# Optimization experiments

Measured on AMD Instinct MI355X. Metric: run time of the kernel, lower is better.

## Reference

```python
import jax, jax.numpy as jnp
import numpy as np

N = 50000      # nodes
E = 500000     # edges (avg degree 10)
D_IN = 256     # input feature dim
HID = 256      # hidden_channels
HEADS = 8
C_HID = HID // HEADS   # 32 per-head dim for concat layers
NCLS = 8               # num_classes (last layer per-head dim, concat=False)


def setup_inputs() -> dict:
    key = jax.random.key(0)
    keys = iter(jax.random.split(key, 64))
    def w(shape, s=0.05):
        return jax.random.normal(next(keys), shape, jnp.float32) * s
    inp = {}
    inp["x"] = jax.random.normal(next(keys), (N, D_IN), jnp.float32)
    inp["edge_index"] = jax.random.randint(next(keys), (2, E), 0, N, jnp.int32)
    # (fan_in, heads*per_head_out, skip_out) per layer; layer3: concat=False
    layer_cfg = [(D_IN, HEADS * C_HID, HEADS * C_HID),
                 (HID, HEADS * C_HID, HEADS * C_HID),
                 (HID, HEADS * NCLS, NCLS)]
    for i, (fin, hc, skip) in enumerate(layer_cfg, 1):
        for nm in ("q", "k", "v"):
            inp[f"W{nm}{i}"] = w((fin, hc))
            inp[f"b{nm}{i}"] = jnp.zeros((hc,), jnp.float32)
        inp[f"Ws{i}"] = w((fin, skip))
        inp[f"bs{i}"] = jnp.zeros((skip,), jnp.float32)
        inp[f"Wb{i}"] = w((3 * skip, 1))
    for i in (1, 2):
        inp[f"ln{i}_g"] = jnp.ones((HID,), jnp.float32)
        inp[f"ln{i}_b"] = jnp.zeros((HID,), jnp.float32)
    return inp


def _layer_norm(x, g, b):
    mu = x.mean(-1, keepdims=True)
    var = ((x - mu) ** 2).mean(-1, keepdims=True)
    return (x - mu) * jax.lax.rsqrt(var + 1e-5) * g + b


def _tconv(x, src, dst, Wq, bq, Wk, bk, Wv, bv, Ws, bs, Wb, concat):
    """PyG TransformerConv with beta=True, root_weight=True, eval-mode (no dropout)."""
    n = x.shape[0]
    q = (x @ Wq + bq).reshape(n, HEADS, -1)   # [N,H,C]
    k = (x @ Wk + bk).reshape(n, HEADS, -1)
    v = (x @ Wv + bv).reshape(n, HEADS, -1)
    C = q.shape[-1]
    # per-edge attention logits, scaled dot product
    logits = (q[dst] * k[src]).sum(-1) * jax.lax.rsqrt(jnp.float32(C))  # [E,H]
    # segment softmax over incoming edges of each dst node
    m = jax.ops.segment_max(logits, dst, num_segments=n)                # [N,H]
    m = jnp.where(jnp.isfinite(m), m, 0.0)                              # empty segments
    e = jnp.exp(logits - m[dst])
    s = jax.ops.segment_sum(e, dst, num_segments=n)
    alpha = e / (s[dst] + 1e-16)                                        # [E,H]
    # scatter-aggregate messages
    out = jax.ops.segment_sum(v[src] * alpha[:, :, None], dst, num_segments=n)  # [N,H,C]
    out = out.reshape(n, -1) if concat else out.mean(axis=1)
    # beta-gated skip connection
    xr = x @ Ws + bs
    beta = jax.nn.sigmoid(jnp.concatenate([out, xr, out - xr], axis=-1) @ Wb)   # [N,1]
    return beta * xr + (1.0 - beta) * out


def reference(x, edge_index,
              Wq1, bq1, Wk1, bk1, Wv1, bv1, Ws1, bs1, Wb1,
              Wq2, bq2, Wk2, bk2, Wv2, bv2, Ws2, bs2, Wb2,
              Wq3, bq3, Wk3, bk3, Wv3, bv3, Ws3, bs3, Wb3,
              ln1_g, ln1_b, ln2_g, ln2_b):
    src, dst = edge_index[0], edge_index[1]
    h = jax.nn.relu(_layer_norm(
        _tconv(x, src, dst, Wq1, bq1, Wk1, bk1, Wv1, bv1, Ws1, bs1, Wb1, True),
        ln1_g, ln1_b))
    h = jax.nn.relu(_layer_norm(
        _tconv(h, src, dst, Wq2, bq2, Wk2, bk2, Wv2, bv2, Ws2, bs2, Wb2, True),
        ln2_g, ln2_b))
    return _tconv(h, src, dst, Wq3, bq3, Wk3, bk3, Wv3, bv3, Ws3, bs3, Wb3, False)
```

## Files before the change

kernel.cpp:

```cpp
#include <hip/hip_runtime.h>
#include <stdint.h>

typedef __attribute__((ext_vector_type(8))) short short8;
typedef __attribute__((ext_vector_type(4))) float f32x4;

struct us4 { unsigned short x, y, z, w; };

__device__ __forceinline__ float b2f(unsigned short u){
  union { unsigned int i; float f; } x; x.i = ((unsigned int)u) << 16; return x.f;
}
__device__ __forceinline__ unsigned short f2b(float f){
  union { float f; unsigned int i; } x; x.f = f;
  unsigned int i = x.i;
  unsigned int r = (i + 0x7FFFu + ((i >> 16) & 1u)) >> 16;
  return (unsigned short)r;
}
__device__ __forceinline__ float sane(float v){
  return fminf(fmaxf(v, -1e30f), 1e30f);
}
__device__ __forceinline__ float lclamp(float v){
  return fminf(fmaxf(v, -60.f), 60.f);
}
__device__ __forceinline__ float ldin(const void* p, size_t i, int f32){
  return f32 ? ((const float*)p)[i] : b2f(((const unsigned short*)p)[i]);
}

__global__ void k_flag(const unsigned short* __restrict__ xu, int* __restrict__ flag){
  __shared__ int cnt;
  if (threadIdx.x == 0) cnt = 0;
  __syncthreads();
  unsigned u = xu[2 * threadIdx.x];
  int e = (u >> 7) & 0xFF;
  if (e >= 97 && e <= 132) atomicAdd(&cnt, 1);
  __syncthreads();
  if (threadIdx.x == 0) flag[0] = (cnt >= 192) ? 0 : 1;
}

__global__ void k_cvt(const void* __restrict__ xin, unsigned short* __restrict__ xb,
                      int n4, const int* __restrict__ flagp){
  int f32 = *flagp;
  int i = blockIdx.x * 256 + threadIdx.x;
  if (i < n4){
    if (f32){
      float4 v = ((const float4*)xin)[i];
      us4 o = { f2b(v.x), f2b(v.y), f2b(v.z), f2b(v.w) };
      ((us4*)xb)[i] = o;
    } else {
      ((us4*)xb)[i] = ((const us4*)xin)[i];
    }
  }
}

__global__ void k_deg(const int* __restrict__ ei, int E, int N, int* __restrict__ deg){
  int e = blockIdx.x * 256 + threadIdx.x;
  if (e < E){
    unsigned d = (unsigned)ei[E + e];
    if (d < (unsigned)N) atomicAdd(&deg[d], 1);
  }
}

__global__ void k_bsum(const int* __restrict__ deg, int N, int* __restrict__ bsum){
  int b = blockIdx.x, t = threadIdx.x;
  int i0 = b * 1024 + t * 4;
  int s = 0;
  if (i0 + 4 <= N){
    int4 v = *(const int4*)&deg[i0];
    s = v.x + v.y + v.z + v.w;
  } else {
    #pragma unroll
    for (int j = 0; j < 4; ++j){ int i = i0 + j; if (i < N) s += deg[i]; }
  }
  #pragma unroll
  for (int off = 32; off; off >>= 1) s += __shfl_xor(s, off);
  __shared__ int ws[4];
  if ((t & 63) == 0) ws[t >> 6] = s;
  __syncthreads();
  if (t == 0) bsum[b] = ws[0] + ws[1] + ws[2] + ws[3];
}

__global__ void k_bscan(const int* __restrict__ bsum, int nb,
                        int* __restrict__ boff, int* __restrict__ rowptr, int N){
  int t = threadIdx.x;
  if (nb <= 64){
    int v = (t < nb) ? bsum[t] : 0;
    int inc = v;
    #pragma unroll
    for (int off = 1; off < 64; off <<= 1){
      int u = __shfl_up(inc, off);
      if (t >= off) inc += u;
    }
    if (t < nb) boff[t] = inc - v;
    if (t == 63) rowptr[N] = inc;
  } else {
    if (t == 0){
      int run = 0;
      for (int i = 0; i < nb; ++i){ boff[i] = run; run += bsum[i]; }
      rowptr[N] = run;
    }
  }
}

__global__ void k_rowptr(const int* __restrict__ deg, const int* __restrict__ boff,
                         int N, int* __restrict__ rowptr, int* __restrict__ cursor){
  int b = blockIdx.x, t = threadIdx.x;
  int i0 = b * 1024 + t * 4;
  int d0 = 0, d1 = 0, d2 = 0, d3 = 0;
  if (i0 + 4 <= N){
    int4 v = *(const int4*)&deg[i0];
    d0 = v.x; d1 = v.y; d2 = v.z; d3 = v.w;
  } else {
    if (i0     < N) d0 = deg[i0];
    if (i0 + 1 < N) d1 = deg[i0 + 1];
    if (i0 + 2 < N) d2 = deg[i0 + 2];
    if (i0 + 3 < N) d3 = deg[i0 + 3];
  }
  int s = d0 + d1 + d2 + d3;
  int lane = t & 63, w = t >> 6;
  int inc = s;
  #pragma unroll
  for (int off = 1; off < 64; off <<= 1){
    int u = __shfl_up(inc, off);
    if (lane >= off) inc += u;
  }
  int wex = inc - s;
  __shared__ int wtot[4];
  if (lane == 63) wtot[w] = inc;
  __syncthreads();
  int cross = 0;
  for (int i = 0; i < w; ++i) cross += wtot[i];
  int basev = boff[b] + cross + wex;
  int r0 = basev, r1 = basev + d0, r2 = r1 + d1, r3 = r2 + d2;
  if (i0 + 4 <= N){
    int4 o = { r0, r1, r2, r3 };
    *(int4*)&rowptr[i0] = o;
    *(int4*)&cursor[i0] = o;
  } else {
    if (i0     < N){ rowptr[i0]   = r0; cursor[i0]   = r0; }
    if (i0 + 1 < N){ rowptr[i0+1] = r1; cursor[i0+1] = r1; }
    if (i0 + 2 < N){ rowptr[i0+2] = r2; cursor[i0+2] = r2; }
    if (i0 + 3 < N){ rowptr[i0+3] = r3; cursor[i0+3] = r3; }
  }
}

__global__ void k_scatter(const int* __restrict__ ei, int E, int N,
                          int* __restrict__ cursor, int* __restrict__ srcs){
  int e = blockIdx.x * 256 + threadIdx.x;
  if (e < E){
    unsigned d = (unsigned)ei[E + e];
    if (d < (unsigned)N){
      int pos = atomicAdd(&cursor[d], 1);
      if ((unsigned)pos < (unsigned)E){
        unsigned s = (unsigned)ei[e];
        srcs[pos] = (s < (unsigned)N) ? (int)s : 0;
      }
    }
  }
}

__global__ void k_pack(const void* __restrict__ Wq, const void* __restrict__ bq,
                       const void* __restrict__ Wk, const void* __restrict__ bk,
                       const void* __restrict__ Wv, const void* __restrict__ bv,
                       const void* __restrict__ Ws, const void* __restrict__ bs,
                       unsigned short* __restrict__ WT, float* __restrict__ bias,
                       int Mq, int Ms, int K, const int* __restrict__ flagp){
  int f32 = *flagp;
  int cg = blockIdx.x;
  int k  = threadIdx.x;
  int mat, c, mc;
  if (cg < 3 * Mq){ mat = cg / Mq; c = cg % Mq; mc = Mq; }
  else if (cg < 3 * Mq + Ms){ mat = 3; c = cg - 3 * Mq; mc = Ms; }
  else { mat = 4; c = 0; mc = 1; }
  const void* W = (mat==0)?Wq:(mat==1)?Wk:(mat==2)?Wv:(mat==3)?Ws:(const void*)0;
  WT[(size_t)cg * K + k] = (mat < 4) ? f2b(ldin(W, (size_t)k * mc + c, f32)) : (unsigned short)0;
  if (k == 0){
    const void* B = (mat==0)?bq:(mat==1)?bk:(mat==2)?bv:(mat==3)?bs:(const void*)0;
    bias[cg] = (mat < 4) ? ldin(B, c, f32) : 0.f;
  }
}

__global__ __launch_bounds__(256) void k_gemm(const unsigned short* __restrict__ A,
                                              const unsigned short* __restrict__ WT,
                                              const float* __restrict__ bias,
                                              unsigned short* __restrict__ B0,
                                              unsigned short* __restrict__ B1,
                                              unsigned short* __restrict__ B2,
                                              unsigned short* __restrict__ B3,
                                              int N, int Mout, int secshift){
  __shared__ __align__(16) unsigned short Alds[64][264];
  __shared__ __align__(16) unsigned short Clds[32][276];
  int tid = threadIdx.x, wid = tid >> 6, lane = tid & 63;
  int l15 = lane & 15, l4 = lane >> 4;
  int row0 = blockIdx.x * 64;
  {
    int srow = tid >> 2, sc4 = tid & 3;
    int ar = row0 + srow; if (ar >= N) ar = N - 1;
    const unsigned short* Ap = A + (size_t)ar * 256;
    #pragma unroll
    for (int i = 0; i < 8; ++i){
      int col = (sc4 + 4 * i) * 8;
      *(short8*)&Alds[srow][col] = *(const short8*)&Ap[col];
    }
  }
  __syncthreads();
  int secw = 1 << secshift;
  int strow = tid >> 3, stchunk = tid & 7;
  for (int cb = wid * 64; cb < Mout; cb += 256){
    f32x4 acc[4][4] = {};
    #pragma unroll
    for (int k0 = 0; k0 < 256; k0 += 32){
      short8 a0 = *(const short8*)&Alds[l15     ][k0 + l4*8];
      short8 a1 = *(const short8*)&Alds[16 + l15][k0 + l4*8];
      short8 a2 = *(const short8*)&Alds[32 + l15][k0 + l4*8];
      short8 a3 = *(const short8*)&Alds[48 + l15][k0 + l4*8];
      const unsigned short* wb = WT + (size_t)(cb + l15) * 256 + k0 + l4*8;
      short8 b0 = *(const short8*)(wb);
      short8 b1 = *(const short8*)(wb + 16*256);
      short8 b2 = *(const short8*)(wb + 32*256);
      short8 b3 = *(const short8*)(wb + 48*256);
      acc[0][0] = __builtin_amdgcn_mfma_f32_16x16x32_bf16(a0, b0, acc[0][0], 0,0,0);
      acc[0][1] = __builtin_amdgcn_mfma_f32_16x16x32_bf16(a0, b1, acc[0][1], 0,0,0);
      acc[0][2] = __builtin_amdgcn_mfma_f32_16x16x32_bf16(a0, b2, acc[0][2], 0,0,0);
      acc[0][3] = __builtin_amdgcn_mfma_f32_16x16x32_bf16(a0, b3, acc[0][3], 0,0,0);
      acc[1][0] = __builtin_amdgcn_mfma_f32_16x16x32_bf16(a1, b0, acc[1][0], 0,0,0);
      acc[1][1] = __builtin_amdgcn_mfma_f32_16x16x32_bf16(a1, b1, acc[1][1], 0,0,0);
      acc[1][2] = __builtin_amdgcn_mfma_f32_16x16x32_bf16(a1, b2, acc[1][2], 0,0,0);
      acc[1][3] = __builtin_amdgcn_mfma_f32_16x16x32_bf16(a1, b3, acc[1][3], 0,0,0);
      acc[2][0] = __builtin_amdgcn_mfma_f32_16x16x32_bf16(a2, b0, acc[2][0], 0,0,0);
      acc[2][1] = __builtin_amdgcn_mfma_f32_16x16x32_bf16(a2, b1, acc[2][1], 0,0,0);
      acc[2][2] = __builtin_amdgcn_mfma_f32_16x16x32_bf16(a2, b2, acc[2][2], 0,0,0);
      acc[2][3] = __builtin_amdgcn_mfma_f32_16x16x32_bf16(a2, b3, acc[2][3], 0,0,0);
      acc[3][0] = __builtin_amdgcn_mfma_f32_16x16x32_bf16(a3, b0, acc[3][0], 0,0,0);
      acc[3][1] = __builtin_amdgcn_mfma_f32_16x16x32_bf16(a3, b1, acc[3][1], 0,0,0);
      acc[3][2] = __builtin_amdgcn_mfma_f32_16x16x32_bf16(a3, b2, acc[3][2], 0,0,0);
      acc[3][3] = __builtin_amdgcn_mfma_f32_16x16x32_bf16(a3, b3, acc[3][3], 0,0,0);
    }
    int gb = cb - wid * 64;
    #pragma unroll
    for (int ph = 0; ph < 2; ++ph){
      #pragma unroll
      for (int rt2 = 0; rt2 < 2; ++rt2){
        int rt = ph*2 + rt2;
        #pragma unroll
        for (int ct = 0; ct < 4; ++ct){
          float bv = bias[cb + ct*16 + l15];
          #pragma unroll
          for (int r = 0; r < 4; ++r)
            Clds[rt2*16 + l4*4 + r][wid*64 + ct*16 + l15] = f2b(acc[rt][ct][r] + bv);
        }
      }
      __syncthreads();
      int grow = row0 + ph*32 + strow;
      if (grow < N){
        int g0 = gb + stchunk * 32;
        int mat = g0 >> secshift;
        int cc  = g0 & (secw - 1);
        unsigned short* Bp = (mat==0)?B0:(mat==1)?B1:(mat==2)?B2:B3;
        unsigned short* dst = Bp + (size_t)grow * secw + cc;
        const unsigned short* srcp = &Clds[strow][stchunk * 32];
        #pragma unroll
        for (int j = 0; j < 4; ++j)
          *(short8*)(dst + j*8) = *(const short8*)(srcp + j*8);
      }
      __syncthreads();
    }
  }
}

__global__ __launch_bounds__(256) void k_attn(const unsigned short* __restrict__ qb,
                                              const unsigned short* __restrict__ kb,
                                              const unsigned short* __restrict__ vb,
                                              const unsigned short* __restrict__ xb,
                                              const int* __restrict__ rowptr,
                                              const int* __restrict__ srcs,
                                              const void* __restrict__ Wb,
                                              const void* __restrict__ lng,
                                              const void* __restrict__ lnb,
                                              unsigned short* __restrict__ hout,
                                              int N, int E, const int* __restrict__ flagp){
  int f32 = *flagp;
  int tid = threadIdx.x, w = tid >> 6, l = tid & 63;
  int n = blockIdx.x * 4 + w;
  if (n >= N) return;
  size_t base = (size_t)n * 256;
  us4 qv = *(const us4*)&qb[base + l*4];
  float q0 = b2f(qv.x), q1 = b2f(qv.y), q2 = b2f(qv.z), q3 = b2f(qv.w);
  int e0 = rowptr[n], e1 = rowptr[n+1];
  if (e0 < 0) e0 = 0;
  if (e1 > E) e1 = E;
  const float scale = 0.17677669529663687f;
  float ss = 0.f, o0 = 0.f, o1 = 0.f, o2 = 0.f, o3 = 0.f;
  int e = e0;
  for (; e + 4 <= e1; e += 4){
    unsigned s0 = (unsigned)srcs[e];   if (s0 >= (unsigned)N) s0 = 0;
    unsigned s1 = (unsigned)srcs[e+1]; if (s1 >= (unsigned)N) s1 = 0;
    unsigned s2 = (unsigned)srcs[e+2]; if (s2 >= (unsigned)N) s2 = 0;
    unsigned s3 = (unsigned)srcs[e+3]; if (s3 >= (unsigned)N) s3 = 0;
    us4 kA = *(const us4*)&kb[(size_t)s0*256 + l*4];
    us4 kB = *(const us4*)&kb[(size_t)s1*256 + l*4];
    us4 kC = *(const us4*)&kb[(size_t)s2*256 + l*4];
    us4 kD = *(const us4*)&kb[(size_t)s3*256 + l*4];
    us4 vA = *(const us4*)&vb[(size_t)s0*256 + l*4];
    us4 vB = *(const us4*)&vb[(size_t)s1*256 + l*4];
    us4 vC = *(const us4*)&vb[(size_t)s2*256 + l*4];
    us4 vD = *(const us4*)&vb[(size_t)s3*256 + l*4];
    float pa = q0*b2f(kA.x) + q1*b2f(kA.y) + q2*b2f(kA.z) + q3*b2f(kA.w);
    float pb = q0*b2f(kB.x) + q1*b2f(kB.y) + q2*b2f(kB.z) + q3*b2f(kB.w);
    float pc = q0*b2f(kC.x) + q1*b2f(kC.y) + q2*b2f(kC.z) + q3*b2f(kC.w);
    float pd = q0*b2f(kD.x) + q1*b2f(kD.y) + q2*b2f(kD.z) + q3*b2f(kD.w);
    pa += __shfl_xor(pa, 1); pa += __shfl_xor(pa, 2); pa += __shfl_xor(pa, 4);
    pb += __shfl_xor(pb, 1); pb += __shfl_xor(pb, 2); pb += __shfl_xor(pb, 4);
    pc += __shfl_xor(pc, 1); pc += __shfl_xor(pc, 2); pc += __shfl_xor(pc, 4);
    pd += __shfl_xor(pd, 1); pd += __shfl_xor(pd, 2); pd += __shfl_xor(pd, 4);
    float ea = __expf(lclamp(pa * scale));
    float eb = __expf(lclamp(pb * scale));
    float ec = __expf(lclamp(pc * scale));
    float ed = __expf(lclamp(pd * scale));
    ss += ea + eb + ec + ed;
    o0 += ea*b2f(vA.x) + eb*b2f(vB.x) + ec*b2f(vC.x) + ed*b2f(vD.x);
    o1 += ea*b2f(vA.y) + eb*b2f(vB.y) + ec*b2f(vC.y) + ed*b2f(vD.y);
    o2 += ea*b2f(vA.z) + eb*b2f(vB.z) + ec*b2f(vC.z) + ed*b2f(vD.z);
    o3 += ea*b2f(vA.w) + eb*b2f(vB.w) + ec*b2f(vC.w) + ed*b2f(vD.w);
  }
  for (; e < e1; ++e){
    unsigned s = (unsigned)srcs[e]; if (s >= (unsigned)N) s = 0;
    us4 kk = *(const us4*)&kb[(size_t)s*256 + l*4];
    us4 vv = *(const us4*)&vb[(size_t)s*256 + l*4];
    float p = q0*b2f(kk.x) + q1*b2f(kk.y) + q2*b2f(kk.z) + q3*b2f(kk.w);
    p += __shfl_xor(p, 1); p += __shfl_xor(p, 2); p += __shfl_xor(p, 4);
    float a = __expf(lclamp(p * scale));
    ss += a;
    o0 += a*b2f(vv.x); o1 += a*b2f(vv.y); o2 += a*b2f(vv.z); o3 += a*b2f(vv.w);
  }
  float sinv = 1.f / (ss + 1e-16f);
  o0 = sane(o0 * sinv); o1 = sane(o1 * sinv);
  o2 = sane(o2 * sinv); o3 = sane(o3 * sinv);
  int c = l * 4;
  us4 xv = *(const us4*)&xb[base + c];
  float x0 = sane(b2f(xv.x)), x1 = sane(b2f(xv.y)), x2 = sane(b2f(xv.z)), x3 = sane(b2f(xv.w));
  float d = o0*ldin(Wb, c+0, f32) + x0*ldin(Wb, 256+c+0, f32) + (o0-x0)*ldin(Wb, 512+c+0, f32)
          + o1*ldin(Wb, c+1, f32) + x1*ldin(Wb, 256+c+1, f32) + (o1-x1)*ldin(Wb, 512+c+1, f32)
          + o2*ldin(Wb, c+2, f32) + x2*ldin(Wb, 256+c+2, f32) + (o2-x2)*ldin(Wb, 512+c+2, f32)
          + o3*ldin(Wb, c+3, f32) + x3*ldin(Wb, 256+c+3, f32) + (o3-x3)*ldin(Wb, 512+c+3, f32);
  #pragma unroll
  for (int off = 32; off; off >>= 1) d += __shfl_xor(d, off);
  float beta = 1.f / (1.f + __expf(-d));
  float r0 = beta*x0 + (1.f-beta)*o0;
  float r1 = beta*x1 + (1.f-beta)*o1;
  float r2 = beta*x2 + (1.f-beta)*o2;
  float r3 = beta*x3 + (1.f-beta)*o3;
  float sm = r0 + r1 + r2 + r3;
  #pragma unroll
  for (int off = 32; off; off >>= 1) sm += __shfl_xor(sm, off);
  float mu = sm * (1.f/256.f);
  float d0 = r0-mu, d1 = r1-mu, d2 = r2-mu, d3 = r3-mu;
  float vv2 = d0*d0 + d1*d1 + d2*d2 + d3*d3;
  #pragma unroll
  for (int off = 32; off; off >>= 1) vv2 += __shfl_xor(vv2, off);
  float rs = rsqrtf(vv2 * (1.f/256.f) + 1e-5f);
  us4 outv;
  outv.x = f2b(fmaxf(d0*rs*ldin(lng,c+0,f32) + ldin(lnb,c+0,f32), 0.f));
  outv.y = f2b(fmaxf(d1*rs*ldin(lng,c+1,f32) + ldin(lnb,c+1,f32), 0.f));
  outv.z = f2b(fmaxf(d2*rs*ldin(lng,c+2,f32) + ldin(lnb,c+2,f32), 0.f));
  outv.w = f2b(fmaxf(d3*rs*ldin(lng,c+3,f32) + ldin(lnb,c+3,f32), 0.f));
  *(us4*)&hout[base + c] = outv;
}

__global__ __launch_bounds__(256) void k_final(const unsigned short* __restrict__ q3,
                                               const unsigned short* __restrict__ k3,
                                               const unsigned short* __restrict__ v3,
                                               const unsigned short* __restrict__ x3,
                                               const int* __restrict__ rowptr,
                                               const int* __restrict__ srcs,
                                               const void* __restrict__ Wb,
                                               void* __restrict__ outp,
                                               int N, int E, const int* __restrict__ flagp){
  int f32 = *flagp;
  int tid = threadIdx.x, w = tid >> 6, l = tid & 63;
  int n = blockIdx.x * 4 + w;
  if (n >= N) return;
  int es = l >> 4, h = (l >> 1) & 7, j = l & 1;
  size_t base = (size_t)n * 64;
  us4 qv = *(const us4*)&q3[base + h*8 + j*4];
  float q0 = b2f(qv.x), q1 = b2f(qv.y), q2 = b2f(qv.z), q3f = b2f(qv.w);
  int e0 = rowptr[n], e1 = rowptr[n+1];
  if (e0 < 0) e0 = 0;
  if (e1 > E) e1 = E;
  int deg = e1 - e0;
  const float scale = 0.35355339059327373f;
  float ss = 0.f, o0 = 0.f, o1 = 0.f, o2 = 0.f, o3 = 0.f;
  for (int ei = es; ei < deg; ei += 4){
    unsigned s = (unsigned)srcs[e0 + ei]; if (s >= (unsigned)N) s = 0;
    us4 kk = *(const us4*)&k3[(size_t)s*64 + h*8 + j*4];
    us4 vv = *(const us4*)&v3[(size_t)s*64 + h*8 + j*4];
    float p = q0*b2f(kk.x) + q1*b2f(kk.y) + q2*b2f(kk.z) + q3f*b2f(kk.w);
    p += __shfl_xor(p, 1);
    float a = __expf(lclamp(p * scale));
    ss += a;
    o0 += a*b2f(vv.x); o1 += a*b2f(vv.y); o2 += a*b2f(vv.z); o3 += a*b2f(vv.w);
  }
  #pragma unroll
  for (int off = 16; off <= 32; off <<= 1){
    ss += __shfl_xor(ss, off);
    o0 += __shfl_xor(o0, off); o1 += __shfl_xor(o1, off);
    o2 += __shfl_xor(o2, off); o3 += __shfl_xor(o3, off);
  }
  float sinv = 1.f / (ss + 1e-16f);
  o0 = sane(o0 * sinv); o1 = sane(o1 * sinv);
  o2 = sane(o2 * sinv); o3 = sane(o3 * sinv);
  #pragma unroll
  for (int off = 2; off <= 8; off <<= 1){
    o0 += __shfl_xor(o0, off); o1 += __shfl_xor(o1, off);
    o2 += __shfl_xor(o2, off); o3 += __shfl_xor(o3, off);
  }
  o0 *= 0.125f; o1 *= 0.125f; o2 *= 0.125f; o3 *= 0.125f;
  us4 xv = *(const us4*)&x3[base + j*4];
  float x0 = sane(b2f(xv.x)), x1 = sane(b2f(xv.y)), x2 = sane(b2f(xv.z)), x3v = sane(b2f(xv.w));
  int c = j*4;
  float d = o0*ldin(Wb, c+0, f32) + x0*ldin(Wb, 8+c+0, f32) + (o0-x0)*ldin(Wb, 16+c+0, f32)
          + o1*ldin(Wb, c+1, f32) + x1*ldin(Wb, 8+c+1, f32) + (o1-x1)*ldin(Wb, 16+c+1, f32)
          + o2*ldin(Wb, c+2, f32) + x2*ldin(Wb, 8+c+2, f32) + (o2-x2)*ldin(Wb, 16+c+2, f32)
          + o3*ldin(Wb, c+3, f32) + x3v*ldin(Wb, 8+c+3, f32) + (o3-x3v)*ldin(Wb, 16+c+3, f32);
  d += __shfl_xor(d, 1);
  float beta = 1.f / (1.f + __expf(-d));
  float r0 = beta*x0  + (1.f-beta)*o0;
  float r1 = beta*x1  + (1.f-beta)*o1;
  float r2 = beta*x2  + (1.f-beta)*o2;
  float r3 = beta*x3v + (1.f-beta)*o3;
  if (l < 2){
    if (f32){
      float* op = (float*)outp + (size_t)n*8 + l*4;
      op[0] = r0; op[1] = r1; op[2] = r2; op[3] = r3;
    } else {
      unsigned short* op = (unsigned short*)outp + (size_t)n*8 + l*4;
      op[0] = f2b(r0); op[1] = f2b(r1); op[2] = f2b(r2); op[3] = f2b(r3);
    }
  }
}

extern "C" void kernel_launch(void* const* d_in, const int* in_sizes, int n_in,
                              void* d_out, int out_size, void* d_ws, size_t ws_size,
                              hipStream_t stream){
  const int* ei = (const int*)d_in[1];
  const int N = in_sizes[0] / 256;
  const int E = in_sizes[1] / 2;

  char* wsp = (char*)d_ws;
  size_t off = 0;
  auto alloc = [&](size_t b) -> void* {
    void* p = wsp + off; off = (off + b + 255) & ~(size_t)255; return p;
  };
  unsigned short* WT1  = (unsigned short*)alloc((size_t)1024*256*2);
  unsigned short* WT2  = (unsigned short*)alloc((size_t)1024*256*2);
  unsigned short* WT3  = (unsigned short*)alloc((size_t)256*256*2);
  float* bias1 = (float*)alloc(1024*4);
  float* bias2 = (float*)alloc(1024*4);
  float* bias3 = (float*)alloc(256*4);
  int* flag   = (int*)alloc(256);
  int* deg    = (int*)alloc((size_t)N*4);
  int* rowptr = (int*)alloc((size_t)(N+1)*4);
  int* cursor = (int*)alloc((size_t)N*4);
  int* bsum   = (int*)alloc(1024*4);
  int* boff   = (int*)alloc(1024*4);
  int* srcs   = (int*)alloc((size_t)E*4);
  unsigned short* xbf = (unsigned short*)alloc((size_t)N*256*2);
  unsigned short* qb  = (unsigned short*)alloc((size_t)N*256*2);
  unsigned short* kb  = (unsigned short*)alloc((size_t)N*256*2);
  unsigned short* vb  = (unsigned short*)alloc((size_t)N*256*2);
  unsigned short* xb  = (unsigned short*)alloc((size_t)N*256*2);
  unsigned short* hbuf= (unsigned short*)alloc((size_t)N*256*2);
  unsigned short* q3 = qb;
  unsigned short* k3 = kb;
  unsigned short* v3 = vb;
  unsigned short* x3 = xb;
  (void)ws_size; (void)n_in; (void)out_size;

  k_flag<<<1, 256, 0, stream>>>((const unsigned short*)d_in[0], flag);
  int n4 = (N * 256) / 4;
  k_cvt<<<(n4 + 255) / 256, 256, 0, stream>>>(d_in[0], xbf, n4, flag);

  hipMemsetAsync(deg, 0, (size_t)N*4, stream);
  int eb = (E + 255) / 256;
  int nbk = (N + 1023) / 1024;
  k_deg<<<eb, 256, 0, stream>>>(ei, E, N, deg);
  k_bsum<<<nbk, 256, 0, stream>>>(deg, N, bsum);
  k_bscan<<<1, 64, 0, stream>>>(bsum, nbk, boff, rowptr, N);
  k_rowptr<<<nbk, 256, 0, stream>>>(deg, boff, N, rowptr, cursor);
  k_scatter<<<eb, 256, 0, stream>>>(ei, E, N, cursor, srcs);

  k_pack<<<1024, 256, 0, stream>>>(d_in[2],  d_in[3],  d_in[4],  d_in[5],  d_in[6],  d_in[7],  d_in[8],  d_in[9],  WT1, bias1, 256, 256, 256, flag);
  k_pack<<<1024, 256, 0, stream>>>(d_in[11], d_in[12], d_in[13], d_in[14], d_in[15], d_in[16], d_in[17], d_in[18], WT2, bias2, 256, 256, 256, flag);
  k_pack<<< 256, 256, 0, stream>>>(d_in[20], d_in[21], d_in[22], d_in[23], d_in[24], d_in[25], d_in[26], d_in[27], WT3, bias3,  64,   8, 256, flag);

  int rb = (N + 63) / 64;
  int nb = (N + 3) / 4;
  k_gemm<<<rb, 256, 0, stream>>>(xbf, WT1, bias1, qb, kb, vb, xb, N, 1024, 8);
  k_attn<<<nb, 256, 0, stream>>>(qb, kb, vb, xb, rowptr, srcs, d_in[10], d_in[29], d_in[30], hbuf, N, E, flag);
  k_gemm<<<rb, 256, 0, stream>>>(hbuf, WT2, bias2, qb, kb, vb, xb, N, 1024, 8);
  k_attn<<<nb, 256, 0, stream>>>(qb, kb, vb, xb, rowptr, srcs, d_in[19], d_in[31], d_in[32], hbuf, N, E, flag);
  k_gemm<<<rb, 256, 0, stream>>>(hbuf, WT3, bias3, q3, k3, v3, x3, N, 256, 6);
  k_final<<<nb, 256, 0, stream>>>(q3, k3, v3, x3, rowptr, srcs, d_in[28], d_out, N, E, flag);
}
```

Baseline: 666.1 us.

## Store QKV projections as fp16 and prescale source indices to byte offsets

The GEMM epilogue now writes q/k/v/skip projections as fp16 instead of bf16, and the attention kernels read them as half4 with native conversion. The CSR scatter stores each source index premultiplied by the row byte stride, so gather addresses become a single add, and the final layer shifts it down for its narrower rows. The layer attention kernel also loads source indices as int4 vectors, unrolls 8 edges per iteration, and adds an occupancy hint to launch bounds. The aim is less per-edge address arithmetic and more memory-level parallelism in the gather. The costs are fp16's narrower range versus bf16, the 32-bit offset limit, and the final layer silently depending on the scaled index encoding.

```diff
diff --git a/kernel.cpp b/kernel.cpp
--- a/kernel.cpp
+++ b/kernel.cpp
@@ -3,6 +3,7 @@
 
 typedef __attribute__((ext_vector_type(8))) short short8;
 typedef __attribute__((ext_vector_type(4))) float f32x4;
+typedef __attribute__((ext_vector_type(4))) _Float16 half4;
 
 struct us4 { unsigned short x, y, z, w; };
 
@@ -14,6 +15,10 @@
   unsigned int i = x.i;
   unsigned int r = (i + 0x7FFFu + ((i >> 16) & 1u)) >> 16;
   return (unsigned short)r;
+}
+__device__ __forceinline__ unsigned short f2h(float f){
+  _Float16 h = (_Float16)f;
+  union { _Float16 h; unsigned short u; } c; c.h = h; return c.u;
 }
 __device__ __forceinline__ float sane(float v){
   return fminf(fmaxf(v, -1e30f), 1e30f);
@@ -151,7 +156,7 @@
       int pos = atomicAdd(&cursor[d], 1);
       if ((unsigned)pos < (unsigned)E){
         unsigned s = (unsigned)ei[e];
-        srcs[pos] = (s < (unsigned)N) ? (int)s : 0;
+        srcs[pos] = (s < (unsigned)N) ? (int)(s * 512u) : 0;
       }
     }
   }
@@ -245,7 +250,7 @@
           float bv = bias[cb + ct*16 + l15];
           #pragma unroll
           for (int r = 0; r < 4; ++r)
-            Clds[rt2*16 + l4*4 + r][wid*64 + ct*16 + l15] = f2b(acc[rt][ct][r] + bv);
+            Clds[rt2*16 + l4*4 + r][wid*64 + ct*16 + l15] = f2h(acc[rt][ct][r] + bv);
         }
       }
       __syncthreads();
@@ -266,77 +271,114 @@
   }
 }
 
-__global__ __launch_bounds__(256) void k_attn(const unsigned short* __restrict__ qb,
-                                              const unsigned short* __restrict__ kb,
-                                              const unsigned short* __restrict__ vb,
-                                              const unsigned short* __restrict__ xb,
-                                              const int* __restrict__ rowptr,
-                                              const int* __restrict__ srcs,
-                                              const void* __restrict__ Wb,
-                                              const void* __restrict__ lng,
-                                              const void* __restrict__ lnb,
-                                              unsigned short* __restrict__ hout,
-                                              int N, int E, const int* __restrict__ flagp){
+__global__ __launch_bounds__(256, 6) void k_attn(const unsigned short* __restrict__ qb,
+                                                 const unsigned short* __restrict__ kb,
+                                                 const unsigned short* __restrict__ vb,
+                                                 const unsigned short* __restrict__ xb,
+                                                 const int* __restrict__ rowptr,
+                                                 const int* __restrict__ srcs,
+                                                 const void* __restrict__ Wb,
+                                                 const void* __restrict__ lng,
+                                                 const void* __restrict__ lnb,
+                                                 unsigned short* __restrict__ hout,
+                                                 int N, int E, const int* __restrict__ flagp){
   int f32 = *flagp;
   int tid = threadIdx.x, w = tid >> 6, l = tid & 63;
   int n = blockIdx.x * 4 + w;
   if (n >= N) return;
-  size_t base = (size_t)n * 256;
-  us4 qv = *(const us4*)&qb[base + l*4];
-  float q0 = b2f(qv.x), q1 = b2f(qv.y), q2 = b2f(qv.z), q3 = b2f(qv.w);
+  const char* q8 = (const char*)qb;
+  const char* k8 = (const char*)kb;
+  const char* v8 = (const char*)vb;
+  const char* x8 = (const char*)xb;
+  unsigned l8 = (unsigned)l * 8u;
+  size_t nbase = (size_t)n * 512;
+  half4 qv = *(const half4*)(q8 + nbase + l8);
+  float q0 = (float)qv.x, q1 = (float)qv.y, q2 = (float)qv.z, q3 = (float)qv.w;
   int e0 = rowptr[n], e1 = rowptr[n+1];
   if (e0 < 0) e0 = 0;
   if (e1 > E) e1 = E;
   const float scale = 0.17677669529663687f;
   float ss = 0.f, o0 = 0.f, o1 = 0.f, o2 = 0.f, o3 = 0.f;
-  int e = e0;
-  for (; e + 4 <= e1; e += 4){
-    unsigned s0 = (unsigned)srcs[e];   if (s0 >= (unsigned)N) s0 = 0;
-    unsigned s1 = (unsigned)srcs[e+1]; if (s1 >= (unsigned)N) s1 = 0;
-    unsigned s2 = (unsigned)srcs[e+2]; if (s2 >= (unsigned)N) s2 = 0;
-    unsigned s3 = (unsigned)srcs[e+3]; if (s3 >= (unsigned)N) s3 = 0;
-    us4 kA = *(const us4*)&kb[(size_t)s0*256 + l*4];
-    us4 kB = *(const us4*)&kb[(size_t)s1*256 + l*4];
-    us4 kC = *(const us4*)&kb[(size_t)s2*256 + l*4];
-    us4 kD = *(const us4*)&kb[(size_t)s3*256 + l*4];
-    us4 vA = *(const us4*)&vb[(size_t)s0*256 + l*4];
-    us4 vB = *(const us4*)&vb[(size_t)s1*256 + l*4];
-    us4 vC = *(const us4*)&vb[(size_t)s2*256 + l*4];
-    us4 vD = *(const us4*)&vb[(size_t)s3*256 + l*4];
-    float pa = q0*b2f(kA.x) + q1*b2f(kA.y) + q2*b2f(kA.z) + q3*b2f(kA.w);
-    float pb = q0*b2f(kB.x) + q1*b2f(kB.y) + q2*b2f(kB.z) + q3*b2f(kB.w);
-    float pc = q0*b2f(kC.x) + q1*b2f(kC.y) + q2*b2f(kC.z) + q3*b2f(kC.w);
-    float pd = q0*b2f(kD.x) + q1*b2f(kD.y) + q2*b2f(kD.z) + q3*b2f(kD.w);
-    pa += __shfl_xor(pa, 1); pa += __shfl_xor(pa, 2); pa += __shfl_xor(pa, 4);
-    pb += __shfl_xor(pb, 1); pb += __shfl_xor(pb, 2); pb += __shfl_xor(pb, 4);
-    pc += __shfl_xor(pc, 1); pc += __shfl_xor(pc, 2); pc += __shfl_xor(pc, 4);
-    pd += __shfl_xor(pd, 1); pd += __shfl_xor(pd, 2); pd += __shfl_xor(pd, 4);
-    float ea = __expf(lclamp(pa * scale));
-    float eb = __expf(lclamp(pb * scale));
-    float ec = __expf(lclamp(pc * scale));
-    float ed = __expf(lclamp(pd * scale));
-    ss += ea + eb + ec + ed;
-    o0 += ea*b2f(vA.x) + eb*b2f(vB.x) + ec*b2f(vC.x) + ed*b2f(vD.x);
-    o1 += ea*b2f(vA.y) + eb*b2f(vB.y) + ec*b2f(vC.y) + ed*b2f(vD.y);
-    o2 += ea*b2f(vA.z) + eb*b2f(vB.z) + ec*b2f(vC.z) + ed*b2f(vD.z);
-    o3 += ea*b2f(vA.w) + eb*b2f(vB.w) + ec*b2f(vC.w) + ed*b2f(vD.w);
-  }
-  for (; e < e1; ++e){
-    unsigned s = (unsigned)srcs[e]; if (s >= (unsigned)N) s = 0;
-    us4 kk = *(const us4*)&kb[(size_t)s*256 + l*4];
-    us4 vv = *(const us4*)&vb[(size_t)s*256 + l*4];
-    float p = q0*b2f(kk.x) + q1*b2f(kk.y) + q2*b2f(kk.z) + q3*b2f(kk.w);
+
+  auto edge1 = [&](int eidx){
+    unsigned off = (unsigned)srcs[eidx] + l8;
+    half4 kk = *(const half4*)(k8 + off);
+    half4 vv = *(const half4*)(v8 + off);
+    float p = q0*(float)kk.x + q1*(float)kk.y + q2*(float)kk.z + q3*(float)kk.w;
     p += __shfl_xor(p, 1); p += __shfl_xor(p, 2); p += __shfl_xor(p, 4);
     float a = __expf(lclamp(p * scale));
     ss += a;
-    o0 += a*b2f(vv.x); o1 += a*b2f(vv.y); o2 += a*b2f(vv.z); o3 += a*b2f(vv.w);
-  }
+    o0 += a*(float)vv.x; o1 += a*(float)vv.y; o2 += a*(float)vv.z; o3 += a*(float)vv.w;
+  };
+
+  int e = e0;
+  while ((e & 3) && e < e1){ edge1(e); ++e; }
+  for (; e + 8 <= e1; e += 8){
+    int4 oA = *(const int4*)&srcs[e];
+    int4 oB = *(const int4*)&srcs[e + 4];
+    unsigned off[8] = { (unsigned)oA.x + l8, (unsigned)oA.y + l8,
+                        (unsigned)oA.z + l8, (unsigned)oA.w + l8,
+                        (unsigned)oB.x + l8, (unsigned)oB.y + l8,
+                        (unsigned)oB.z + l8, (unsigned)oB.w + l8 };
+    half4 kk[8], vv[8];
+    #pragma unroll
+    for (int j = 0; j < 8; ++j) kk[j] = *(const half4*)(k8 + off[j]);
+    #pragma unroll
+    for (int j = 0; j < 8; ++j) vv[j] = *(const half4*)(v8 + off[j]);
+    float p[8];
+    #pragma unroll
+    for (int j = 0; j < 8; ++j)
+      p[j] = q0*(float)kk[j].x + q1*(float)kk[j].y + q2*(float)kk[j].z + q3*(float)kk[j].w;
+    #pragma unroll
+    for (int j = 0; j < 8; ++j){
+      p[j] += __shfl_xor(p[j], 1);
+      p[j] += __shfl_xor(p[j], 2);
+      p[j] += __shfl_xor(p[j], 4);
+    }
+    #pragma unroll
+    for (int j = 0; j < 8; ++j){
+      float a = __expf(lclamp(p[j] * scale));
+      ss += a;
+      o0 += a*(float)vv[j].x; o1 += a*(float)vv[j].y;
+      o2 += a*(float)vv[j].z; o3 += a*(float)vv[j].w;
+    }
+  }
+  for (; e + 4 <= e1; e += 4){
+    int4 oA = *(const int4*)&srcs[e];
+    unsigned off[4] = { (unsigned)oA.x + l8, (unsigned)oA.y + l8,
+                        (unsigned)oA.z + l8, (unsigned)oA.w + l8 };
+    half4 kk[4], vv[4];
+    #pragma unroll
+    for (int j = 0; j < 4; ++j) kk[j] = *(const half4*)(k8 + off[j]);
+    #pragma unroll
+    for (int j = 0; j < 4; ++j) vv[j] = *(const half4*)(v8 + off[j]);
+    float p[4];
+    #pragma unroll
+    for (int j = 0; j < 4; ++j)
+      p[j] = q0*(float)kk[j].x + q1*(float)kk[j].y + q2*(float)kk[j].z + q3*(float)kk[j].w;
+    #pragma unroll
+    for (int j = 0; j < 4; ++j){
+      p[j] += __shfl_xor(p[j], 1);
+      p[j] += __shfl_xor(p[j], 2);
+      p[j] += __shfl_xor(p[j], 4);
+    }
+    #pragma unroll
+    for (int j = 0; j < 4; ++j){
+      float a = __expf(lclamp(p[j] * scale));
+      ss += a;
+      o0 += a*(float)vv[j].x; o1 += a*(float)vv[j].y;
+      o2 += a*(float)vv[j].z; o3 += a*(float)vv[j].w;
+    }
+  }
+  for (; e < e1; ++e) edge1(e);
+
   float sinv = 1.f / (ss + 1e-16f);
   o0 = sane(o0 * sinv); o1 = sane(o1 * sinv);
   o2 = sane(o2 * sinv); o3 = sane(o3 * sinv);
   int c = l * 4;
-  us4 xv = *(const us4*)&xb[base + c];
-  float x0 = sane(b2f(xv.x)), x1 = sane(b2f(xv.y)), x2 = sane(b2f(xv.z)), x3 = sane(b2f(xv.w));
+  half4 xv = *(const half4*)(x8 + nbase + l8);
+  float x0 = sane((float)xv.x), x1 = sane((float)xv.y);
+  float x2 = sane((float)xv.z), x3 = sane((float)xv.w);
   float d = o0*ldin(Wb, c+0, f32) + x0*ldin(Wb, 256+c+0, f32) + (o0-x0)*ldin(Wb, 512+c+0, f32)
           + o1*ldin(Wb, c+1, f32) + x1*ldin(Wb, 256+c+1, f32) + (o1-x1)*ldin(Wb, 512+c+1, f32)
           + o2*ldin(Wb, c+2, f32) + x2*ldin(Wb, 256+c+2, f32) + (o2-x2)*ldin(Wb, 512+c+2, f32)
@@ -362,13 +404,13 @@
   outv.y = f2b(fmaxf(d1*rs*ldin(lng,c+1,f32) + ldin(lnb,c+1,f32), 0.f));
   outv.z = f2b(fmaxf(d2*rs*ldin(lng,c+2,f32) + ldin(lnb,c+2,f32), 0.f));
   outv.w = f2b(fmaxf(d3*rs*ldin(lng,c+3,f32) + ldin(lnb,c+3,f32), 0.f));
-  *(us4*)&hout[base + c] = outv;
-}
-
-__global__ __launch_bounds__(256) void k_final(const unsigned short* __restrict__ q3,
-                                               const unsigned short* __restrict__ k3,
-                                               const unsigned short* __restrict__ v3,
-                                               const unsigned short* __restrict__ x3,
+  *(us4*)&hout[(size_t)n * 256 + c] = outv;
+}
+
+__global__ __launch_bounds__(256) void k_final(const unsigned short* __restrict__ q3b,
+                                               const unsigned short* __restrict__ k3b,
+                                               const unsigned short* __restrict__ v3b,
+                                               const unsigned short* __restrict__ x3b,
                                                const int* __restrict__ rowptr,
                                                const int* __restrict__ srcs,
                                                const void* __restrict__ Wb,
@@ -379,24 +421,49 @@
   int n = blockIdx.x * 4 + w;
   if (n >= N) return;
   int es = l >> 4, h = (l >> 1) & 7, j = l & 1;
-  size_t base = (size_t)n * 64;
-  us4 qv = *(const us4*)&q3[base + h*8 + j*4];
-  float q0 = b2f(qv.x), q1 = b2f(qv.y), q2 = b2f(qv.z), q3f = b2f(qv.w);
+  unsigned sub = (unsigned)(h * 16 + j * 8);
+  const char* q8 = (const char*)q3b;
+  const char* k8 = (const char*)k3b;
+  const char* v8 = (const char*)v3b;
+  const char* x8 = (const char*)x3b;
+  size_t nbase = (size_t)n * 128;
+  half4 qv = *(const half4*)(q8 + nbase + sub);
+  float q0 = (float)qv.x, q1 = (float)qv.y, q2 = (float)qv.z, q3f = (float)qv.w;
   int e0 = rowptr[n], e1 = rowptr[n+1];
   if (e0 < 0) e0 = 0;
   if (e1 > E) e1 = E;
   int deg = e1 - e0;
   const float scale = 0.35355339059327373f;
   float ss = 0.f, o0 = 0.f, o1 = 0.f, o2 = 0.f, o3 = 0.f;
-  for (int ei = es; ei < deg; ei += 4){
-    unsigned s = (unsigned)srcs[e0 + ei]; if (s >= (unsigned)N) s = 0;
-    us4 kk = *(const us4*)&k3[(size_t)s*64 + h*8 + j*4];
-    us4 vv = *(const us4*)&v3[(size_t)s*64 + h*8 + j*4];
-    float p = q0*b2f(kk.x) + q1*b2f(kk.y) + q2*b2f(kk.z) + q3f*b2f(kk.w);
+  int ei = es;
+  for (; ei + 4 < deg; ei += 8){
+    unsigned offA = (((unsigned)srcs[e0 + ei])     >> 2) + sub;
+    unsigned offB = (((unsigned)srcs[e0 + ei + 4]) >> 2) + sub;
+    half4 kA = *(const half4*)(k8 + offA);
+    half4 vA = *(const half4*)(v8 + offA);
+    half4 kB = *(const half4*)(k8 + offB);
+    half4 vB = *(const half4*)(v8 + offB);
+    float pA = q0*(float)kA.x + q1*(float)kA.y + q2*(float)kA.z + q3f*(float)kA.w;
+    float pB = q0*(float)kB.x + q1*(float)kB.y + q2*(float)kB.z + q3f*(float)kB.w;
+    pA += __shfl_xor(pA, 1);
+    pB += __shfl_xor(pB, 1);
+    float aA = __expf(lclamp(pA * scale));
+    float aB = __expf(lclamp(pB * scale));
+    ss += aA + aB;
+    o0 += aA*(float)vA.x + aB*(float)vB.x;
+    o1 += aA*(float)vA.y + aB*(float)vB.y;
+    o2 += aA*(float)vA.z + aB*(float)vB.z;
+    o3 += aA*(float)vA.w + aB*(float)vB.w;
+  }
+  if (ei < deg){
+    unsigned off = (((unsigned)srcs[e0 + ei]) >> 2) + sub;
+    half4 kk = *(const half4*)(k8 + off);
+    half4 vv = *(const half4*)(v8 + off);
+    float p = q0*(float)kk.x + q1*(float)kk.y + q2*(float)kk.z + q3f*(float)kk.w;
     p += __shfl_xor(p, 1);
     float a = __expf(lclamp(p * scale));
     ss += a;
-    o0 += a*b2f(vv.x); o1 += a*b2f(vv.y); o2 += a*b2f(vv.z); o3 += a*b2f(vv.w);
+    o0 += a*(float)vv.x; o1 += a*(float)vv.y; o2 += a*(float)vv.z; o3 += a*(float)vv.w;
   }
   #pragma unroll
   for (int off = 16; off <= 32; off <<= 1){
@@ -413,8 +480,9 @@
     o2 += __shfl_xor(o2, off); o3 += __shfl_xor(o3, off);
   }
   o0 *= 0.125f; o1 *= 0.125f; o2 *= 0.125f; o3 *= 0.125f;
-  us4 xv = *(const us4*)&x3[base + j*4];
-  float x0 = sane(b2f(xv.x)), x1 = sane(b2f(xv.y)), x2 = sane(b2f(xv.z)), x3v = sane(b2f(xv.w));
+  half4 xv = *(const half4*)(x8 + nbase + (unsigned)(j * 8));
+  float x0 = sane((float)xv.x), x1 = sane((float)xv.y);
+  float x2 = sane((float)xv.z), x3v = sane((float)xv.w);
   int c = j*4;
   float d = o0*ldin(Wb, c+0, f32) + x0*ldin(Wb, 8+c+0, f32) + (o0-x0)*ldin(Wb, 16+c+0, f32)
           + o1*ldin(Wb, c+1, f32) + x1*ldin(Wb, 8+c+1, f32) + (o1-x1)*ldin(Wb, 16+c+1, f32)
```

Result: no change. 671.2 us (+0.8%).
